# Optimization experiments

Measured on AMD Instinct MI355X. Metric: run time of the kernel, lower is better.

## Reference

```python
import jax, jax.numpy as jnp
import numpy as np

B, N, D = 16, 2048, 128  # batch, nodes, embedding_dim

def setup_inputs() -> dict:
    key = jax.random.key(0)
    ks = jax.random.split(key, 12)
    def dense(kw, kb, din, dout):
        # keras Dense default glorot_uniform weight, zeros bias (use small random bias for generality)
        lim = np.sqrt(6.0 / (din + dout))
        W = jax.random.uniform(kw, (din, dout), minval=-lim, maxval=lim, dtype=jnp.float32)
        b = jax.random.normal(kb, (dout,), dtype=jnp.float32) * 0.01
        return W, b
    Wq, bq = dense(ks[0], ks[1], D, D)
    Wk, bk = dense(ks[2], ks[3], D, D)
    Wv, bv = dense(ks[4], ks[5], D, D)
    Wo, bo = dense(ks[6], ks[7], D, D)
    query_ = jax.random.normal(ks[8], (B, N, D), dtype=jnp.float32)
    key_ = jax.random.normal(ks[9], (B, N, D), dtype=jnp.float32)
    mask = jax.random.randint(ks[10], (B, N + 1, N + 1), 0, 2).astype(bool)
    return {"query_": query_, "key_": key_, "mask": mask,
            "Wq": Wq, "bq": bq, "Wk": Wk, "bk": bk,
            "Wv": Wv, "bv": bv, "Wo": Wo, "bo": bo}

def reference(query_, key_, mask, Wq, bq, Wk, bk, Wv, bv, Wo, bo):
    q = query_ @ Wq + bq                       # [B,N,D]
    k = key_ @ Wk + bk                         # [B,N,D]
    comp = jnp.einsum('bqd,bkd->bqk', q, k)    # [B,N,N]
    comp = comp / jnp.sqrt(jnp.asarray(k.shape[-1], jnp.float32))
    m = mask[:, 1:, 1:]                        # [B,N,N]
    comp = jnp.where(m, -jnp.inf, comp)
    attn = jax.nn.softmax(comp, axis=-1)
    attn = jnp.where(jnp.isnan(attn), 0.0, attn)  # fully-masked rows -> 0
    # NOTE: faithful to source: value projection applied to the PROJECTED key
    v = k @ Wv + bv                            # [B,N,D]
    out = jnp.einsum('bqk,bkd->bqd', attn, v)
    return out @ Wo + bo
```

## Files before the change

### kernel.cpp

```cpp
#include <hip/hip_runtime.h>

#define SB 16
#define SN 2048
#define SD 128
#define NM 2049
#define SZ (SB*SN*SD)

typedef __bf16 bf16x8 __attribute__((ext_vector_type(8)));
typedef float f32x4 __attribute__((ext_vector_type(4)));

__device__ __forceinline__ unsigned short f2b(float f){
  union { float f; unsigned int u; } v; v.f = f;
  unsigned int r = v.u + 0x7fffu + ((v.u >> 16) & 1u);
  return (unsigned short)(r >> 16);
}

__device__ __forceinline__ void async16(const void* g, void* l){
  __builtin_amdgcn_global_load_lds(
      (__attribute__((address_space(1))) void*)(g),
      (__attribute__((address_space(3))) void*)(l), 16, 0, 0);
}

__global__ __launch_bounds__(256) void prep_w_kernel(
    const float* __restrict__ Wq, const float* __restrict__ Wk,
    const float* __restrict__ Wv, const float* __restrict__ Wo,
    unsigned short* __restrict__ out)
{
  int widx = blockIdx.x >> 4;
  int kg   = blockIdx.x & 15;
  const float* W = (widx==0)?Wq:(widx==1)?Wk:(widx==2)?Wv:Wo;
  unsigned short* O = out + widx*16384;
  int t = threadIdx.x;
  int k = kg*8 + (t>>5);
  int n = (t&31)*4;
  float4 v = *reinterpret_cast<const float4*>(W + k*SD + n);
  O[(n+0)*SD + k] = f2b(v.x);
  O[(n+1)*SD + k] = f2b(v.y);
  O[(n+2)*SD + k] = f2b(v.z);
  O[(n+3)*SD + k] = f2b(v.w);
}

__global__ __launch_bounds__(256) void prep_wkv_kernel(
    const float* __restrict__ Wk, const float* __restrict__ Wv,
    const float* __restrict__ bk, const float* __restrict__ bv,
    unsigned short* __restrict__ WkvT, float* __restrict__ bkv)
{
  int t = threadIdx.x;
  int k = blockIdx.x*8 + (t>>5);
  int n0 = (t&31)*4;
  float ax=0.f, ay=0.f, az=0.f, aw=0.f;
  for (int m=0;m<SD;m++){
    float wk = Wk[k*SD+m];
    float4 wv = *reinterpret_cast<const float4*>(Wv + m*SD + n0);
    ax += wk*wv.x; ay += wk*wv.y; az += wk*wv.z; aw += wk*wv.w;
  }
  WkvT[(n0+0)*SD + k] = f2b(ax);
  WkvT[(n0+1)*SD + k] = f2b(ay);
  WkvT[(n0+2)*SD + k] = f2b(az);
  WkvT[(n0+3)*SD + k] = f2b(aw);
  if (blockIdx.x==0 && t < SD){
    float a = 0.f;
    for (int m=0;m<SD;m++) a += bk[m]*Wv[m*SD + t];
    bkv[t] = a + bv[t];
  }
}

__global__ __launch_bounds__(256,4) void qkv_kernel(
    const float* __restrict__ query, const float* __restrict__ key,
    const unsigned short* __restrict__ wts,
    const float* __restrict__ bq, const float* __restrict__ bk,
    const float* __restrict__ bkv,
    unsigned short* __restrict__ qb, unsigned short* __restrict__ kb,
    unsigned short* __restrict__ vt)
{
  int tid=threadIdx.x;
  int w=tid>>6, ln=tid&63, g=ln>>4, lm=ln&15;
  int wr = (w + ((blockIdx.x & 1) << 1)) & 3;
  int id = blockIdx.x*2 + (wr & 1);
  int b = id >> 7, nt = id & 127;
  size_t rowbase = (size_t)b*SN + nt*16;

  if (wr < 2){
    const unsigned short* WkT  = wts + 16384;
    const unsigned short* WkvT = wts + 32768;
    const float* xr = key + (rowbase + lm)*SD;
    bf16x8 af[4];
    for (int ks=0;ks<4;ks++){
      float4 x0 = *reinterpret_cast<const float4*>(xr + ks*32 + g*8);
      float4 x1 = *reinterpret_cast<const float4*>(xr + ks*32 + g*8 + 4);
      union { bf16x8 v; unsigned short s[8]; } u;
      u.s[0]=f2b(x0.x); u.s[1]=f2b(x0.y); u.s[2]=f2b(x0.z); u.s[3]=f2b(x0.w);
      u.s[4]=f2b(x1.x); u.s[5]=f2b(x1.y); u.s[6]=f2b(x1.z); u.s[7]=f2b(x1.w);
      af[ks]=u.v;
    }
    for (int d=0; d<8; d++){
      f32x4 acc = {0.f,0.f,0.f,0.f};
      for (int ks=0;ks<4;ks++){
        bf16x8 wf = *reinterpret_cast<const bf16x8*>(WkT + (d*16+lm)*SD + ks*32 + g*8);
        acc = __builtin_amdgcn_mfma_f32_16x16x32_bf16(af[ks], wf, acc, 0,0,0);
      }
      float bb = bk[d*16+lm];
      for (int r=0;r<4;r++)
        kb[(rowbase + 4*g + r)*SD + d*16 + lm] = f2b(acc[r]+bb);
    }
    unsigned short* vcol = vt + (size_t)b*SD*SN + nt*16 + lm;
    for (int d=0; d<8; d++){
      f32x4 acc = {0.f,0.f,0.f,0.f};
      for (int ks=0;ks<4;ks++){
        bf16x8 wf = *reinterpret_cast<const bf16x8*>(WkvT + (d*16+lm)*SD + ks*32 + g*8);
        acc = __builtin_amdgcn_mfma_f32_16x16x32_bf16(wf, af[ks], acc, 0,0,0);
      }
      float4 bb = *reinterpret_cast<const float4*>(bkv + d*16 + 4*g);
      vcol[(size_t)(d*16 + 4*g + 0)*SN] = f2b(acc[0]+bb.x);
      vcol[(size_t)(d*16 + 4*g + 1)*SN] = f2b(acc[1]+bb.y);
      vcol[(size_t)(d*16 + 4*g + 2)*SN] = f2b(acc[2]+bb.z);
      vcol[(size_t)(d*16 + 4*g + 3)*SN] = f2b(acc[3]+bb.w);
    }
  } else {
    const unsigned short* WqT = wts;
    const float sc = 0.08838834764831845f;
    const float* xr = query + (rowbase + lm)*SD;
    bf16x8 af[4];
    for (int ks=0;ks<4;ks++){
      float4 x0 = *reinterpret_cast<const float4*>(xr + ks*32 + g*8);
      float4 x1 = *reinterpret_cast<const float4*>(xr + ks*32 + g*8 + 4);
      union { bf16x8 v; unsigned short s[8]; } u;
      u.s[0]=f2b(x0.x); u.s[1]=f2b(x0.y); u.s[2]=f2b(x0.z); u.s[3]=f2b(x0.w);
      u.s[4]=f2b(x1.x); u.s[5]=f2b(x1.y); u.s[6]=f2b(x1.z); u.s[7]=f2b(x1.w);
      af[ks]=u.v;
    }
    for (int d=0; d<8; d++){
      f32x4 acc = {0.f,0.f,0.f,0.f};
      for (int ks=0;ks<4;ks++){
        bf16x8 wf = *reinterpret_cast<const bf16x8*>(WqT + (d*16+lm)*SD + ks*32 + g*8);
        acc = __builtin_amdgcn_mfma_f32_16x16x32_bf16(af[ks], wf, acc, 0,0,0);
      }
      float bb = bq[d*16+lm];
      for (int r=0;r<4;r++)
        qb[(rowbase + 4*g + r)*SD + d*16 + lm] = f2b((acc[r]+bb)*sc);
    }
  }
}

__global__ __launch_bounds__(256,4) void flash_kernel(
    const unsigned short* __restrict__ qb, const unsigned short* __restrict__ kb,
    const unsigned short* __restrict__ vt, const int* __restrict__ mask,
    const unsigned short* __restrict__ WoT, const float* __restrict__ bo,
    float* __restrict__ out)
{
  __shared__ unsigned short bufK[2][64*128];
  __shared__ unsigned short bufV[2][128*64];
  __shared__ unsigned short ldsP[4*16*72];

  int tid=threadIdx.x;
  int w=tid>>6, ln=tid&63, g=ln>>4, lm=ln&15;
  int xcd   = blockIdx.x & 7;
  int inner = blockIdx.x >> 3;
  int b  = xcd*2 + (inner>>5);
  int qt = inner & 31;
  int q0 = qt*64;

  const unsigned short* Qb = qb + (size_t)b*SN*SD;
  const unsigned short* Kb = kb + (size_t)b*SN*SD;
  const unsigned short* Vb = vt + (size_t)b*SD*SN;
  const int* Mb = mask + (size_t)b*NM*NM;

  auto issueK = [&](int k0, int bi){
    const char* gbase = (const char*)Kb + (size_t)k0*256;
    for (int c=0;c<4;c++){
      int p = c*256 + tid;
      int row = p>>4, lc = (p&15) ^ (row&15);
      async16(gbase + (size_t)row*256 + lc*16, (char*)bufK[bi] + p*16);
    }
  };
  auto issueV = [&](int k0, int bi){
    const char* gbase = (const char*)Vb + (size_t)k0*2;
    for (int c=0;c<4;c++){
      int p = c*256 + tid;
      int row = p>>3, lc = (p&7) ^ (row&7);
      async16(gbase + (size_t)row*4096 + lc*16, (char*)bufV[bi] + p*16);
    }
  };

  issueK(0,0); issueV(0,0);

  bf16x8 qf[4];
  {
    const unsigned short* qr = Qb + (size_t)(q0 + w*16 + lm)*SD;
    for (int ks=0;ks<4;ks++)
      qf[ks] = *reinterpret_cast<const bf16x8*>(qr + ks*32 + g*8);
  }

  int qr1 = 1 + q0 + w*16 + 4*g;
  const int* mbase = Mb + (size_t)qr1*NM + 1 + lm;
  int mreg[16];
  for (int ct=0;ct<4;ct++)
    for (int r=0;r<4;r++)
      mreg[ct*4+r] = __builtin_nontemporal_load(mbase + (size_t)r*NM + ct*16);

  float mrow[4], lrow[4], al[4];
  f32x4 acc[8];
  for (int r=0;r<4;r++){ mrow[r]=-INFINITY; lrow[r]=0.f; }
  for (int d=0;d<8;d++){ f32x4 z={0.f,0.f,0.f,0.f}; acc[d]=z; }
  unsigned short* pw = &ldsP[w*16*72];

  for (int kt=0; kt<32; kt++){
    __syncthreads();
    int cur = kt&1;
    if (kt<31){ issueK((kt+1)*64, cur^1); issueV((kt+1)*64, cur^1); }

    f32x4 s[4];
    __builtin_amdgcn_s_setprio(1);
    for (int ct=0;ct<4;ct++){
      f32x4 z = {0.f,0.f,0.f,0.f};
      for (int ks=0;ks<4;ks++){
        bf16x8 kf = *reinterpret_cast<const bf16x8*>(
            &bufK[cur][(ct*16+lm)*128 + (((ks*4+g)^lm))*8]);
        z = __builtin_amdgcn_mfma_f32_16x16x32_bf16(qf[ks], kf, z, 0,0,0);
      }
      s[ct]=z;
    }
    __builtin_amdgcn_s_setprio(0);

    for (int ct=0;ct<4;ct++)
      for (int r=0;r<4;r++)
        s[ct][r] = mreg[ct*4+r] ? -INFINITY : s[ct][r];
    if (kt<31){
      const int* mp = mbase + (kt+1)*64;
      for (int ct=0;ct<4;ct++)
        for (int r=0;r<4;r++)
          mreg[ct*4+r] = __builtin_nontemporal_load(mp + (size_t)r*NM + ct*16);
    }

    for (int r=0;r<4;r++){
      float v = fmaxf(fmaxf(s[0][r],s[1][r]), fmaxf(s[2][r],s[3][r]));
      v = fmaxf(v, __shfl_xor(v,1,16));
      v = fmaxf(v, __shfl_xor(v,2,16));
      v = fmaxf(v, __shfl_xor(v,4,16));
      v = fmaxf(v, __shfl_xor(v,8,16));
      float mn = fmaxf(mrow[r], v);
      bool dead = (mn == -INFINITY);
      float a = dead ? 1.f : __expf(mrow[r]-mn);
      float rsum = 0.f;
      for (int ct=0;ct<4;ct++){
        float p = dead ? 0.f : __expf(s[ct][r]-mn);
        s[ct][r]=p; rsum += p;
      }
      rsum += __shfl_xor(rsum,1,16);
      rsum += __shfl_xor(rsum,2,16);
      rsum += __shfl_xor(rsum,4,16);
      rsum += __shfl_xor(rsum,8,16);
      lrow[r] = lrow[r]*a + rsum;
      mrow[r] = mn;
      al[r] = a;
    }
    for (int d=0;d<8;d++)
      for (int r=0;r<4;r++)
        acc[d][r] *= al[r];

    for (int ct=0;ct<4;ct++){
      int col = ct*16+lm;
      for (int r=0;r<4;r++)
        pw[(4*g+r)*72 + col] = f2b(s[ct][r]);
    }
    bf16x8 pa0 = *reinterpret_cast<const bf16x8*>(&pw[lm*72 + g*8]);
    bf16x8 pa1 = *reinterpret_cast<const bf16x8*>(&pw[lm*72 + 32 + g*8]);

    __builtin_amdgcn_s_setprio(1);
    for (int d=0;d<8;d++){
      bf16x8 v0 = *reinterpret_cast<const bf16x8*>(
          &bufV[cur][(d*16+lm)*64 + ((g^(lm&7)))*8]);
      acc[d] = __builtin_amdgcn_mfma_f32_16x16x32_bf16(pa0, v0, acc[d], 0,0,0);
      bf16x8 v1 = *reinterpret_cast<const bf16x8*>(
          &bufV[cur][(d*16+lm)*64 + (((4+g)^(lm&7)))*8]);
      acc[d] = __builtin_amdgcn_mfma_f32_16x16x32_bf16(pa1, v1, acc[d], 0,0,0);
    }
    __builtin_amdgcn_s_setprio(0);
  }

  __syncthreads();
  float inv[4];
  for (int r=0;r<4;r++) inv[r] = (lrow[r] > 0.f) ? (1.f/lrow[r]) : 0.f;
  unsigned short* strip = &bufK[0][0] + w*2176;
  for (int d=0;d<8;d++)
    for (int r=0;r<4;r++)
      strip[(4*g+r)*136 + d*16 + lm] = f2b(acc[d][r]*inv[r]);
  bf16x8 oa[4];
  for (int ks=0;ks<4;ks++)
    oa[ks] = *reinterpret_cast<const bf16x8*>(&strip[lm*136 + ks*32 + g*8]);
  float* Ob = out + ((size_t)b*SN + q0 + w*16)*SD;
  for (int dc=0; dc<8; dc++){
    f32x4 o = {0.f,0.f,0.f,0.f};
    for (int ks=0;ks<4;ks++){
      bf16x8 wf = *reinterpret_cast<const bf16x8*>(WoT + (dc*16+lm)*SD + ks*32 + g*8);
      o = __builtin_amdgcn_mfma_f32_16x16x32_bf16(oa[ks], wf, o, 0,0,0);
    }
    float bb = bo[dc*16+lm];
    for (int r=0;r<4;r++)
      __builtin_nontemporal_store(o[r]+bb, &Ob[(size_t)(4*g+r)*SD + dc*16 + lm]);
  }
}

extern "C" void kernel_launch(void* const* d_in, const int* in_sizes, int n_in,
                              void* d_out, int out_size, void* d_ws, size_t ws_size,
                              hipStream_t stream)
{
  const float* query = (const float*)d_in[0];
  const float* key   = (const float*)d_in[1];
  const int*   mask  = (const int*)d_in[2];
  const float* Wq = (const float*)d_in[3];
  const float* bq = (const float*)d_in[4];
  const float* Wk = (const float*)d_in[5];
  const float* bk = (const float*)d_in[6];
  const float* Wv = (const float*)d_in[7];
  const float* bv = (const float*)d_in[8];
  const float* Wo = (const float*)d_in[9];
  const float* bo = (const float*)d_in[10];
  float* out = (float*)d_out;

  unsigned short* qb = (unsigned short*)d_ws;
  unsigned short* kb = qb + SZ;
  unsigned short* vt = kb + SZ;
  unsigned short* wts = vt + SZ;
  float* bkv = (float*)(wts + 65536);

  prep_w_kernel  <<<64,256,0,stream>>>(Wq,Wk,Wv,Wo,wts);
  prep_wkv_kernel<<<16,256,0,stream>>>(Wk,Wv,bk,bv, wts+32768, bkv);
  qkv_kernel     <<<1024,256,0,stream>>>(query, key, wts, bq, bk, bkv, qb, kb, vt);
  flash_kernel   <<<512,256,0,stream>>>(qb, kb, vt, mask, wts+49152, bo, out);
}
```

Before: 500.7 us.

## Pack attention mask into bitmasks in projection kernel and stage V transpose via LDS

The QKV projection kernel gains extra blocks that read the int32 mask once and pack each row into 64-bit ballot bitmasks. The flash kernel then reads these compact bits instead of 16 scattered int loads per tile. The V transpose is also staged through shared memory so global writes become coalesced 16-byte stores. Mask bandwidth shifts into the projection kernel, which now runs 3072 blocks, and the mask bits must be extracted per element with shifts.

```diff
diff --git a/kernel.cpp b/kernel.cpp
--- a/kernel.cpp
+++ b/kernel.cpp
@@ -8,6 +8,7 @@
 
 typedef __bf16 bf16x8 __attribute__((ext_vector_type(8)));
 typedef float f32x4 __attribute__((ext_vector_type(4)));
+typedef unsigned long long u64;
 
 __device__ __forceinline__ unsigned short f2b(float f){
   union { float f; unsigned int u; } v; v.f = f;
@@ -65,22 +66,42 @@
   }
 }
 
-__global__ __launch_bounds__(256,4) void qkv_kernel(
+__global__ __launch_bounds__(256,4) void qkv_pack_kernel(
     const float* __restrict__ query, const float* __restrict__ key,
+    const int* __restrict__ mask,
     const unsigned short* __restrict__ wts,
     const float* __restrict__ bq, const float* __restrict__ bk,
     const float* __restrict__ bkv,
     unsigned short* __restrict__ qb, unsigned short* __restrict__ kb,
-    unsigned short* __restrict__ vt)
-{
+    unsigned short* __restrict__ vt, u64* __restrict__ pmask)
+{
+  __shared__ unsigned short vT[128*72];
+
   int tid=threadIdx.x;
   int w=tid>>6, ln=tid&63, g=ln>>4, lm=ln&15;
-  int wr = (w + ((blockIdx.x & 1) << 1)) & 3;
-  int id = blockIdx.x*2 + (wr & 1);
-  int b = id >> 7, nt = id & 127;
-  size_t rowbase = (size_t)b*SN + nt*16;
-
-  if (wr < 2){
+  int bi = blockIdx.x;
+
+  if (bi >= 1024){
+    int pid = bi - 1024;
+    for (int rr=0; rr<4; rr++){
+      int row = pid*16 + w*4 + rr;
+      int b = row >> 11, qr = row & 2047;
+      const int* src = mask + (size_t)b*NM*NM + (size_t)(1+qr)*NM + 1;
+      u64* dst = pmask + (size_t)row*32;
+      for (int i=0;i<32;i++){
+        int m = __builtin_nontemporal_load(src + i*64 + ln);
+        u64 bal = __ballot(m != 0);
+        if (ln == 0) dst[i] = bal;
+      }
+    }
+    return;
+  }
+
+  int id = bi >> 1;
+  int b = id >> 5, nt = id & 31;
+  size_t rowbase = (size_t)b*SN + nt*64 + w*16;
+
+  if ((bi & 1) == 0){
     const unsigned short* WkT  = wts + 16384;
     const unsigned short* WkvT = wts + 32768;
     const float* xr = key + (rowbase + lm)*SD;
@@ -103,7 +124,6 @@
       for (int r=0;r<4;r++)
         kb[(rowbase + 4*g + r)*SD + d*16 + lm] = f2b(acc[r]+bb);
     }
-    unsigned short* vcol = vt + (size_t)b*SD*SN + nt*16 + lm;
     for (int d=0; d<8; d++){
       f32x4 acc = {0.f,0.f,0.f,0.f};
       for (int ks=0;ks<4;ks++){
@@ -111,11 +131,16 @@
         acc = __builtin_amdgcn_mfma_f32_16x16x32_bf16(wf, af[ks], acc, 0,0,0);
       }
       float4 bb = *reinterpret_cast<const float4*>(bkv + d*16 + 4*g);
-      vcol[(size_t)(d*16 + 4*g + 0)*SN] = f2b(acc[0]+bb.x);
-      vcol[(size_t)(d*16 + 4*g + 1)*SN] = f2b(acc[1]+bb.y);
-      vcol[(size_t)(d*16 + 4*g + 2)*SN] = f2b(acc[2]+bb.z);
-      vcol[(size_t)(d*16 + 4*g + 3)*SN] = f2b(acc[3]+bb.w);
-    }
+      vT[(d*16 + 4*g + 0)*72 + w*16 + lm] = f2b(acc[0]+bb.x);
+      vT[(d*16 + 4*g + 1)*72 + w*16 + lm] = f2b(acc[1]+bb.y);
+      vT[(d*16 + 4*g + 2)*72 + w*16 + lm] = f2b(acc[2]+bb.z);
+      vT[(d*16 + 4*g + 3)*72 + w*16 + lm] = f2b(acc[3]+bb.w);
+    }
+    __syncthreads();
+    int d = tid>>1, half = tid&1;
+    const uint4* src4 = reinterpret_cast<const uint4*>(&vT[d*72 + half*32]);
+    uint4* dst4 = reinterpret_cast<uint4*>(vt + (size_t)b*SD*SN + (size_t)d*SN + nt*64 + half*32);
+    dst4[0]=src4[0]; dst4[1]=src4[1]; dst4[2]=src4[2]; dst4[3]=src4[3];
   } else {
     const unsigned short* WqT = wts;
     const float sc = 0.08838834764831845f;
@@ -144,7 +169,7 @@
 
 __global__ __launch_bounds__(256,4) void flash_kernel(
     const unsigned short* __restrict__ qb, const unsigned short* __restrict__ kb,
-    const unsigned short* __restrict__ vt, const int* __restrict__ mask,
+    const unsigned short* __restrict__ vt, const u64* __restrict__ pmask,
     const unsigned short* __restrict__ WoT, const float* __restrict__ bo,
     float* __restrict__ out)
 {
@@ -163,7 +188,6 @@
   const unsigned short* Qb = qb + (size_t)b*SN*SD;
   const unsigned short* Kb = kb + (size_t)b*SN*SD;
   const unsigned short* Vb = vt + (size_t)b*SD*SN;
-  const int* Mb = mask + (size_t)b*NM*NM;
 
   auto issueK = [&](int k0, int bi){
     const char* gbase = (const char*)Kb + (size_t)k0*256;
@@ -191,12 +215,10 @@
       qf[ks] = *reinterpret_cast<const bf16x8*>(qr + ks*32 + g*8);
   }
 
-  int qr1 = 1 + q0 + w*16 + 4*g;
-  const int* mbase = Mb + (size_t)qr1*NM + 1 + lm;
-  int mreg[16];
-  for (int ct=0;ct<4;ct++)
-    for (int r=0;r<4;r++)
-      mreg[ct*4+r] = __builtin_nontemporal_load(mbase + (size_t)r*NM + ct*16);
+  const u64* pmb = pmask + ((size_t)(b*2048 + q0 + w*16 + 4*g))*32;
+  u64 mb[4];
+#pragma unroll
+  for (int r=0;r<4;r++) mb[r] = pmb[r*32];
 
   float mrow[4], lrow[4], al[4];
   f32x4 acc[8];
@@ -222,14 +244,19 @@
     }
     __builtin_amdgcn_s_setprio(0);
 
-    for (int ct=0;ct<4;ct++)
-      for (int r=0;r<4;r++)
-        s[ct][r] = mreg[ct*4+r] ? -INFINITY : s[ct][r];
+#pragma unroll
+    for (int ct=0;ct<4;ct++){
+      unsigned wlo, sh;
+#pragma unroll
+      for (int r=0;r<4;r++){
+        if (ct < 2){ wlo = (unsigned)mb[r];        sh = ct*16 + lm; }
+        else       { wlo = (unsigned)(mb[r]>>32);  sh = (ct-2)*16 + lm; }
+        if ((wlo >> sh) & 1u) s[ct][r] = -INFINITY;
+      }
+    }
     if (kt<31){
-      const int* mp = mbase + (kt+1)*64;
-      for (int ct=0;ct<4;ct++)
-        for (int r=0;r<4;r++)
-          mreg[ct*4+r] = __builtin_nontemporal_load(mp + (size_t)r*NM + ct*16);
+#pragma unroll
+      for (int r=0;r<4;r++) mb[r] = pmb[r*32 + kt + 1];
     }
 
     for (int r=0;r<4;r++){
@@ -323,9 +350,11 @@
   unsigned short* vt = kb + SZ;
   unsigned short* wts = vt + SZ;
   float* bkv = (float*)(wts + 65536);
+  u64* pmask = (u64*)(bkv + 128);
 
   prep_w_kernel  <<<64,256,0,stream>>>(Wq,Wk,Wv,Wo,wts);
   prep_wkv_kernel<<<16,256,0,stream>>>(Wk,Wv,bk,bv, wts+32768, bkv);
-  qkv_kernel     <<<1024,256,0,stream>>>(query, key, wts, bq, bk, bkv, qb, kb, vt);
-  flash_kernel   <<<512,256,0,stream>>>(qb, kb, vt, mask, wts+49152, bo, out);
-}
+  qkv_pack_kernel<<<3072,256,0,stream>>>(query, key, mask, wts, bq, bk, bkv,
+                                         qb, kb, vt, pmask);
+  flash_kernel   <<<512,256,0,stream>>>(qb, kb, vt, pmask, wts+49152, bo, out);
+}
```

Result: slower. 601.5 us (+20.1%).

## Process two query strips per flash block and stage QKV stores through LDS

Applied to the files above, without the earlier changes.

The flash kernel now handles 128 query rows per block as two 64-row strips that share each K/V tile loaded into LDS. This halves global K/V traffic and halves the grid to 256 blocks, at the cost of doubled accumulator registers and lower occupancy via launch_bounds(256,2). The QKV kernel also stages K, Q and transposed V outputs in LDS so it can write coalesced 16-byte stores instead of scattered 2-byte column writes. One blocking change is that fewer blocks are in flight (256 on a large GPU), which may leave compute units idle.

```diff
diff --git a/kernel.cpp b/kernel.cpp
--- a/kernel.cpp
+++ b/kernel.cpp
@@ -73,14 +73,20 @@
     unsigned short* __restrict__ qb, unsigned short* __restrict__ kb,
     unsigned short* __restrict__ vt)
 {
+  __shared__ unsigned short vT[128*72];
+  __shared__ unsigned short kq[4][16*136];
+
   int tid=threadIdx.x;
   int w=tid>>6, ln=tid&63, g=ln>>4, lm=ln&15;
-  int wr = (w + ((blockIdx.x & 1) << 1)) & 3;
-  int id = blockIdx.x*2 + (wr & 1);
-  int b = id >> 7, nt = id & 127;
-  size_t rowbase = (size_t)b*SN + nt*16;
-
-  if (wr < 2){
+  int bi = blockIdx.x;
+
+  int id = bi >> 1;
+  int b = id >> 5, nt = id & 31;
+  size_t rowbase = (size_t)b*SN + nt*64 + w*16;
+  unsigned short* st = &kq[w][0];
+  int srow = ln>>2, sqtr = ln&3;
+
+  if ((bi & 1) == 0){
     const unsigned short* WkT  = wts + 16384;
     const unsigned short* WkvT = wts + 32768;
     const float* xr = key + (rowbase + lm)*SD;
@@ -101,9 +107,14 @@
       }
       float bb = bk[d*16+lm];
       for (int r=0;r<4;r++)
-        kb[(rowbase + 4*g + r)*SD + d*16 + lm] = f2b(acc[r]+bb);
-    }
-    unsigned short* vcol = vt + (size_t)b*SD*SN + nt*16 + lm;
+        st[(4*g+r)*136 + d*16 + lm] = f2b(acc[r]+bb);
+    }
+    asm volatile("" ::: "memory");
+    {
+      const uint4* s4 = reinterpret_cast<const uint4*>(&st[srow*136 + sqtr*32]);
+      uint4* d4 = reinterpret_cast<uint4*>(kb + (rowbase + srow)*SD + sqtr*32);
+      d4[0]=s4[0]; d4[1]=s4[1]; d4[2]=s4[2]; d4[3]=s4[3];
+    }
     for (int d=0; d<8; d++){
       f32x4 acc = {0.f,0.f,0.f,0.f};
       for (int ks=0;ks<4;ks++){
@@ -111,11 +122,16 @@
         acc = __builtin_amdgcn_mfma_f32_16x16x32_bf16(wf, af[ks], acc, 0,0,0);
       }
       float4 bb = *reinterpret_cast<const float4*>(bkv + d*16 + 4*g);
-      vcol[(size_t)(d*16 + 4*g + 0)*SN] = f2b(acc[0]+bb.x);
-      vcol[(size_t)(d*16 + 4*g + 1)*SN] = f2b(acc[1]+bb.y);
-      vcol[(size_t)(d*16 + 4*g + 2)*SN] = f2b(acc[2]+bb.z);
-      vcol[(size_t)(d*16 + 4*g + 3)*SN] = f2b(acc[3]+bb.w);
-    }
+      vT[(d*16 + 4*g + 0)*72 + w*16 + lm] = f2b(acc[0]+bb.x);
+      vT[(d*16 + 4*g + 1)*72 + w*16 + lm] = f2b(acc[1]+bb.y);
+      vT[(d*16 + 4*g + 2)*72 + w*16 + lm] = f2b(acc[2]+bb.z);
+      vT[(d*16 + 4*g + 3)*72 + w*16 + lm] = f2b(acc[3]+bb.w);
+    }
+    __syncthreads();
+    int d = tid>>1, half = tid&1;
+    const uint4* src4 = reinterpret_cast<const uint4*>(&vT[d*72 + half*32]);
+    uint4* dst4 = reinterpret_cast<uint4*>(vt + (size_t)b*SD*SN + (size_t)d*SN + nt*64 + half*32);
+    dst4[0]=src4[0]; dst4[1]=src4[1]; dst4[2]=src4[2]; dst4[3]=src4[3];
   } else {
     const unsigned short* WqT = wts;
     const float sc = 0.08838834764831845f;
@@ -137,12 +153,18 @@
       }
       float bb = bq[d*16+lm];
       for (int r=0;r<4;r++)
-        qb[(rowbase + 4*g + r)*SD + d*16 + lm] = f2b((acc[r]+bb)*sc);
-    }
-  }
-}
-
-__global__ __launch_bounds__(256,4) void flash_kernel(
+        st[(4*g+r)*136 + d*16 + lm] = f2b((acc[r]+bb)*sc);
+    }
+    asm volatile("" ::: "memory");
+    {
+      const uint4* s4 = reinterpret_cast<const uint4*>(&st[srow*136 + sqtr*32]);
+      uint4* d4 = reinterpret_cast<uint4*>(qb + (rowbase + srow)*SD + sqtr*32);
+      d4[0]=s4[0]; d4[1]=s4[1]; d4[2]=s4[2]; d4[3]=s4[3];
+    }
+  }
+}
+
+__global__ __launch_bounds__(256,2) void flash_kernel(
     const unsigned short* __restrict__ qb, const unsigned short* __restrict__ kb,
     const unsigned short* __restrict__ vt, const int* __restrict__ mask,
     const unsigned short* __restrict__ WoT, const float* __restrict__ bo,
@@ -150,15 +172,15 @@
 {
   __shared__ unsigned short bufK[2][64*128];
   __shared__ unsigned short bufV[2][128*64];
-  __shared__ unsigned short ldsP[4*16*72];
+  __shared__ unsigned short ldsP[4][16*72];
 
   int tid=threadIdx.x;
   int w=tid>>6, ln=tid&63, g=ln>>4, lm=ln&15;
   int xcd   = blockIdx.x & 7;
   int inner = blockIdx.x >> 3;
-  int b  = xcd*2 + (inner>>5);
-  int qt = inner & 31;
-  int q0 = qt*64;
+  int b  = xcd*2 + (inner>>4);
+  int qt = inner & 15;
+  int q0 = qt*128;
 
   const unsigned short* Qb = qb + (size_t)b*SN*SD;
   const unsigned short* Kb = kb + (size_t)b*SN*SD;
@@ -170,7 +192,7 @@
     for (int c=0;c<4;c++){
       int p = c*256 + tid;
       int row = p>>4, lc = (p&15) ^ (row&15);
-      async16(gbase + (size_t)row*256 + lc*16, (char*)bufK[bi] + p*16);
+      async16(gbase + (size_t)row*256 + lc*16, (char*)(&bufK[bi][0]) + p*16);
     }
   };
   auto issueV = [&](int k0, int bi){
@@ -178,37 +200,40 @@
     for (int c=0;c<4;c++){
       int p = c*256 + tid;
       int row = p>>3, lc = (p&7) ^ (row&7);
-      async16(gbase + (size_t)row*4096 + lc*16, (char*)bufV[bi] + p*16);
+      async16(gbase + (size_t)row*4096 + lc*16, (char*)(&bufV[bi][0]) + p*16);
     }
   };
 
   issueK(0,0); issueV(0,0);
 
-  bf16x8 qf[4];
+  bf16x8 qf0[4], qf1[4];
   {
-    const unsigned short* qr = Qb + (size_t)(q0 + w*16 + lm)*SD;
-    for (int ks=0;ks<4;ks++)
-      qf[ks] = *reinterpret_cast<const bf16x8*>(qr + ks*32 + g*8);
-  }
-
-  int qr1 = 1 + q0 + w*16 + 4*g;
-  const int* mbase = Mb + (size_t)qr1*NM + 1 + lm;
-  int mreg[16];
+    const unsigned short* qr0 = Qb + (size_t)(q0 + w*16 + lm)*SD;
+    const unsigned short* qr1 = qr0 + (size_t)64*SD;
+    for (int ks=0;ks<4;ks++){
+      qf0[ks] = *reinterpret_cast<const bf16x8*>(qr0 + ks*32 + g*8);
+      qf1[ks] = *reinterpret_cast<const bf16x8*>(qr1 + ks*32 + g*8);
+    }
+  }
+
+  const int* mb0 = Mb + (size_t)(1 + q0 + w*16 + 4*g)*NM + 1 + lm;
+  const int* mb1 = mb0 + (size_t)64*NM;
+  int mr0[16], mr1[16];
   for (int ct=0;ct<4;ct++)
-    for (int r=0;r<4;r++)
-      mreg[ct*4+r] = __builtin_nontemporal_load(mbase + (size_t)r*NM + ct*16);
-
-  float mrow[4], lrow[4], al[4];
-  f32x4 acc[8];
-  for (int r=0;r<4;r++){ mrow[r]=-INFINITY; lrow[r]=0.f; }
-  for (int d=0;d<8;d++){ f32x4 z={0.f,0.f,0.f,0.f}; acc[d]=z; }
-  unsigned short* pw = &ldsP[w*16*72];
-
-  for (int kt=0; kt<32; kt++){
-    __syncthreads();
-    int cur = kt&1;
-    if (kt<31){ issueK((kt+1)*64, cur^1); issueV((kt+1)*64, cur^1); }
-
+    for (int r=0;r<4;r++){
+      mr0[ct*4+r] = __builtin_nontemporal_load(mb0 + (size_t)r*NM + ct*16);
+      mr1[ct*4+r] = __builtin_nontemporal_load(mb1 + (size_t)r*NM + ct*16);
+    }
+
+  float mrow0[4], lrow0[4], mrow1[4], lrow1[4];
+  f32x4 acc0[8], acc1[8];
+  for (int r=0;r<4;r++){ mrow0[r]=-INFINITY; lrow0[r]=0.f; mrow1[r]=-INFINITY; lrow1[r]=0.f; }
+  for (int d=0;d<8;d++){ f32x4 z={0.f,0.f,0.f,0.f}; acc0[d]=z; acc1[d]=z; }
+  unsigned short* pw = &ldsP[w][0];
+
+  auto strip = [&](bf16x8 (&qf)[4], int (&mreg)[16], float (&mrow)[4],
+                   float (&lrow)[4], f32x4 (&acc)[8], const int* mnext,
+                   int cur, bool pf){
     f32x4 s[4];
     __builtin_amdgcn_s_setprio(1);
     for (int ct=0;ct<4;ct++){
@@ -225,13 +250,13 @@
     for (int ct=0;ct<4;ct++)
       for (int r=0;r<4;r++)
         s[ct][r] = mreg[ct*4+r] ? -INFINITY : s[ct][r];
-    if (kt<31){
-      const int* mp = mbase + (kt+1)*64;
+    if (pf){
       for (int ct=0;ct<4;ct++)
         for (int r=0;r<4;r++)
-          mreg[ct*4+r] = __builtin_nontemporal_load(mp + (size_t)r*NM + ct*16);
-    }
-
+          mreg[ct*4+r] = __builtin_nontemporal_load(mnext + (size_t)r*NM + ct*16);
+    }
+
+    float al[4];
     for (int r=0;r<4;r++){
       float v = fmaxf(fmaxf(s[0][r],s[1][r]), fmaxf(s[2][r],s[3][r]));
       v = fmaxf(v, __shfl_xor(v,1,16));
@@ -263,8 +288,10 @@
       for (int r=0;r<4;r++)
         pw[(4*g+r)*72 + col] = f2b(s[ct][r]);
     }
+    asm volatile("" ::: "memory");
     bf16x8 pa0 = *reinterpret_cast<const bf16x8*>(&pw[lm*72 + g*8]);
     bf16x8 pa1 = *reinterpret_cast<const bf16x8*>(&pw[lm*72 + 32 + g*8]);
+    asm volatile("" ::: "memory");
 
     __builtin_amdgcn_s_setprio(1);
     for (int d=0;d<8;d++){
@@ -276,29 +303,44 @@
       acc[d] = __builtin_amdgcn_mfma_f32_16x16x32_bf16(pa1, v1, acc[d], 0,0,0);
     }
     __builtin_amdgcn_s_setprio(0);
+  };
+
+  for (int kt=0; kt<32; kt++){
+    __syncthreads();
+    int cur = kt&1;
+    if (kt<31){ issueK((kt+1)*64, cur^1); issueV((kt+1)*64, cur^1); }
+    strip(qf0, mr0, mrow0, lrow0, acc0, mb0 + (size_t)(kt+1)*64, cur, kt<31);
+    strip(qf1, mr1, mrow1, lrow1, acc1, mb1 + (size_t)(kt+1)*64, cur, kt<31);
   }
 
   __syncthreads();
-  float inv[4];
-  for (int r=0;r<4;r++) inv[r] = (lrow[r] > 0.f) ? (1.f/lrow[r]) : 0.f;
-  unsigned short* strip = &bufK[0][0] + w*2176;
-  for (int d=0;d<8;d++)
-    for (int r=0;r<4;r++)
-      strip[(4*g+r)*136 + d*16 + lm] = f2b(acc[d][r]*inv[r]);
-  bf16x8 oa[4];
-  for (int ks=0;ks<4;ks++)
-    oa[ks] = *reinterpret_cast<const bf16x8*>(&strip[lm*136 + ks*32 + g*8]);
-  float* Ob = out + ((size_t)b*SN + q0 + w*16)*SD;
-  for (int dc=0; dc<8; dc++){
-    f32x4 o = {0.f,0.f,0.f,0.f};
-    for (int ks=0;ks<4;ks++){
-      bf16x8 wf = *reinterpret_cast<const bf16x8*>(WoT + (dc*16+lm)*SD + ks*32 + g*8);
-      o = __builtin_amdgcn_mfma_f32_16x16x32_bf16(oa[ks], wf, o, 0,0,0);
-    }
-    float bb = bo[dc*16+lm];
-    for (int r=0;r<4;r++)
-      __builtin_nontemporal_store(o[r]+bb, &Ob[(size_t)(4*g+r)*SD + dc*16 + lm]);
-  }
+  auto epi = [&](f32x4 (&acc)[8], float (&lrow)[4], int soff){
+    float inv[4];
+    for (int r=0;r<4;r++) inv[r] = (lrow[r] > 0.f) ? (1.f/lrow[r]) : 0.f;
+    unsigned short* strip_ = &bufK[0][0] + w*2176;
+    for (int d=0;d<8;d++)
+      for (int r=0;r<4;r++)
+        strip_[(4*g+r)*136 + d*16 + lm] = f2b(acc[d][r]*inv[r]);
+    asm volatile("" ::: "memory");
+    bf16x8 oa[4];
+    for (int ks=0;ks<4;ks++)
+      oa[ks] = *reinterpret_cast<const bf16x8*>(&strip_[lm*136 + ks*32 + g*8]);
+    asm volatile("" ::: "memory");
+    float* Ob = out + ((size_t)b*SN + q0 + soff + w*16)*SD;
+    for (int dc=0; dc<8; dc++){
+      f32x4 o = {0.f,0.f,0.f,0.f};
+      for (int ks=0;ks<4;ks++){
+        bf16x8 wf = *reinterpret_cast<const bf16x8*>(WoT + (dc*16+lm)*SD + ks*32 + g*8);
+        o = __builtin_amdgcn_mfma_f32_16x16x32_bf16(oa[ks], wf, o, 0,0,0);
+      }
+      float bb = bo[dc*16+lm];
+      for (int r=0;r<4;r++)
+        __builtin_nontemporal_store(o[r]+bb, &Ob[(size_t)(4*g+r)*SD + dc*16 + lm]);
+    }
+    asm volatile("" ::: "memory");
+  };
+  epi(acc0, lrow0, 0);
+  epi(acc1, lrow1, 64);
 }
 
 extern "C" void kernel_launch(void* const* d_in, const int* in_sizes, int n_in,
@@ -327,5 +369,5 @@
   prep_w_kernel  <<<64,256,0,stream>>>(Wq,Wk,Wv,Wo,wts);
   prep_wkv_kernel<<<16,256,0,stream>>>(Wk,Wv,bk,bv, wts+32768, bkv);
   qkv_kernel     <<<1024,256,0,stream>>>(query, key, wts, bq, bk, bkv, qb, kb, vt);
-  flash_kernel   <<<512,256,0,stream>>>(qb, kb, vt, mask, wts+49152, bo, out);
-}
+  flash_kernel   <<<256,256,0,stream>>>(qb, kb, vt, mask, wts+49152, bo, out);
+}
```

Result: slower. 516.7 us (+3.2%).
